# Kernel optimization log

Measured on AMD Instinct MI355X. Metric: run time of the kernel, lower is better.

## Reference

```python
import jax, jax.numpy as jnp
import numpy as np

H = 64  # rnn_size == input_size

def setup_inputs() -> dict:
    key = jax.random.key(0)
    ks = jax.random.split(key, 6)
    vocab = 32000
    B, T = 4096, 128
    s = 1.0 / np.sqrt(H)
    return {
        "inst": jax.random.randint(ks[0], (B, T), 0, vocab, dtype=jnp.int64),
        "embed_w": jax.random.normal(ks[1], (vocab + 1, H), dtype=jnp.float32),
        "W_ih": jax.random.uniform(ks[2], (4 * H, H), dtype=jnp.float32, minval=-s, maxval=s),
        "W_hh": jax.random.uniform(ks[3], (4 * H, H), dtype=jnp.float32, minval=-s, maxval=s),
        "b_ih": jax.random.uniform(ks[4], (4 * H,), dtype=jnp.float32, minval=-s, maxval=s),
        "b_hh": jax.random.uniform(ks[5], (4 * H,), dtype=jnp.float32, minval=-s, maxval=s),
    }

def _lstm_scan(xs, W_ih, W_hh, b_ih, b_hh):
    # xs: [T, B, H]. PyTorch LSTMCell gate order: i, f, g, o.
    B = xs.shape[1]
    # Precompute input projections for all timesteps in one big GEMM.
    x_proj = jnp.einsum('tbh,gh->tbg', xs, W_ih) + b_ih + b_hh  # [T, B, 4H]

    def step(carry, xp):
        h, c = carry
        gates = xp + h @ W_hh.T  # [B, 4H]
        i, f, g, o = jnp.split(gates, 4, axis=-1)
        c = jax.nn.sigmoid(f) * c + jax.nn.sigmoid(i) * jnp.tanh(g)
        h = jax.nn.sigmoid(o) * jnp.tanh(c)
        return (h, c), None

    h0 = jnp.zeros((B, H), dtype=xs.dtype)
    c0 = jnp.zeros((B, H), dtype=xs.dtype)
    (h, c), _ = jax.lax.scan(step, (h0, c0), x_proj)
    return h

def reference(inst, embed_w, W_ih, W_hh, b_ih, b_hh):
    # inst: [B, T] int; embedding lookup for whole sequence at once.
    xs = embed_w[inst]                 # [B, T, H]
    xs = jnp.swapaxes(xs, 0, 1)        # [T, B, H] for scan over time
    return _lstm_scan(xs, W_ih, W_hh, b_ih, b_hh)  # final h: [B, H]
```

## Files before the change

### kernel.cpp

```cpp
#include <hip/hip_runtime.h>
#include <hip/hip_bf16.h>

#define H_DIM   64
#define T_STEPS 128
#define B_TOT   4096
#define BB      8
#define SK      72
#define NTHREADS 256
#define XBATCH  8

typedef _Float16 half8  __attribute__((ext_vector_type(8)));
typedef __fp16   fp16x2 __attribute__((ext_vector_type(2)));
typedef __attribute__((ext_vector_type(4))) float f32x4;

#if __has_builtin(__builtin_amdgcn_exp2f)
#define EXP2(x) __builtin_amdgcn_exp2f(x)
#else
#define EXP2(x) exp2f(x)
#endif

__device__ __forceinline__ float sigmoid2(float xp) {
    return __builtin_amdgcn_rcpf(1.0f + EXP2(-xp));
}
__device__ __forceinline__ float tanh2(float xp) {
    return fmaf(-2.0f, __builtin_amdgcn_rcpf(EXP2(xp) + 1.0f), 1.0f);
}

__device__ __forceinline__ float xor8_dpp(float v) {
    return __int_as_float(__builtin_amdgcn_mov_dpp(
        __float_as_int(v), 0x128 , 0xf, 0xf, false));
}

__global__ __launch_bounds__(NTHREADS) void lstm_fused(
    const int* __restrict__ inst, const float* __restrict__ embed,
    const float* __restrict__ Wih, const float* __restrict__ Whh,
    const float* __restrict__ bih, const float* __restrict__ bhh,
    float* __restrict__ out)
{
    __shared__ __align__(16) _Float16 sX[2][16][SK];
    __shared__ __align__(16) _Float16 sH[2][16][SK];
    __shared__ int sInst[BB * T_STEPS];

    const int tid  = (int)threadIdx.x;
    const int w    = tid >> 6;
    const int l    = tid & 63;
    const int lrow = l & 15;
    const int lk   = l >> 4;
    const bool losd = (lrow < 8);
    const int colbase = w * 16 + (lrow & 7);
    const int rstar = losd ? 0 : 1;
    const int mrow  = lk * 4 + rstar;
    const int br    = lk * 2 + rstar;
    const int b0    = (int)blockIdx.x * BB;

    const float L2E     = 1.4426950408889634f;
    const float TWO_L2E = 2.8853900817779268f;

    for (int i = tid; i < BB * T_STEPS; i += NTHREADS)
        sInst[i] = inst[b0 * T_STEPS + i];

    for (int i = tid; i < 2 * 16 * SK; i += NTHREADS) {
        ((_Float16*)sX)[i] = (_Float16)0.0f;
        ((_Float16*)sH)[i] = (_Float16)0.0f;
    }
    __syncthreads();

    half8 wf[2][2][4];
    float bias[2][2];
#pragma unroll
    for (int cg = 0; cg < 2; ++cg) {
#pragma unroll
        for (int q = 0; q < 2; ++q) {
            const int gate = q * 2 + (lrow >> 3);
            const float ws = (gate == 2) ? TWO_L2E : L2E;
            const int gcol = gate * 64 + colbase + cg * 8;
            bias[cg][q] = (bih[gcol] + bhh[gcol]) * ws;
#pragma unroll
            for (int kf = 0; kf < 4; ++kf) {
                const float* src = (kf < 2 ? Wih : Whh) + (long)gcol * H_DIM + (kf & 1) * 32 + lk * 8;
                half8 v;
#pragma unroll
                for (int jj = 0; jj < 8; ++jj) v[jj] = (_Float16)(src[jj] * ws);
                wf[cg][q][kf] = v;
            }
        }
    }

    const int xr = tid >> 5;
    const int xc = tid & 31;
    const int xm = (xr >> 1) * 4 + (xr & 1);
    {
        const int idx = sInst[xr * T_STEPS + 0];
        const float2 xv = *reinterpret_cast<const float2*>(embed + (long)idx * H_DIM + xc * 2);
        fp16x2 hp = __builtin_amdgcn_cvt_pkrtz(xv.x, xv.y);
        *reinterpret_cast<fp16x2*>(&sX[0][xm][xc * 2]) = hp;
    }

    float2 xbuf[XBATCH];
#pragma unroll
    for (int j = 0; j < XBATCH; ++j) {
        const int idx = sInst[xr * T_STEPS + 1 + j];
        xbuf[j] = *reinterpret_cast<const float2*>(embed + (long)idx * H_DIM + xc * 2);
    }
    __syncthreads();

    float creg[2] = {0.f, 0.f};
    float hreg[2] = {0.f, 0.f};

    for (int tb = 0; tb < T_STEPS; tb += XBATCH) {
#pragma unroll
        for (int j = 0; j < XBATCH; ++j) {
            const int t   = tb + j;
            const int buf = j & 1;
            const int ob  = buf ^ 1;
            const bool pf = (t + 1 < T_STEPS);

            const float2 xcur = xbuf[j];

            if (j == XBATCH - 1 && pf) {
#pragma unroll
                for (int jj = 0; jj < XBATCH; ++jj) {
                    const int tt = t + 2 + jj;
                    if (tt < T_STEPS) {
                        const int idx = sInst[xr * T_STEPS + tt];
                        xbuf[jj] = *reinterpret_cast<const float2*>(embed + (long)idx * H_DIM + xc * 2);
                    }
                }
            }

            half8 a0 = *reinterpret_cast<const half8*>(&sX[buf][lrow][lk * 8]);
            half8 a1 = *reinterpret_cast<const half8*>(&sX[buf][lrow][32 + lk * 8]);
            half8 a2 = *reinterpret_cast<const half8*>(&sH[buf][lrow][lk * 8]);
            half8 a3 = *reinterpret_cast<const half8*>(&sH[buf][lrow][32 + lk * 8]);

            f32x4 acc[2][2];
#pragma unroll
            for (int cg = 0; cg < 2; ++cg) {
#pragma unroll
                for (int q = 0; q < 2; ++q) {
                    f32x4 a = {bias[cg][q], bias[cg][q], bias[cg][q], bias[cg][q]};
                    a = __builtin_amdgcn_mfma_f32_16x16x32_f16(a0, wf[cg][q][0], a, 0, 0, 0);
                    a = __builtin_amdgcn_mfma_f32_16x16x32_f16(a1, wf[cg][q][1], a, 0, 0, 0);
                    a = __builtin_amdgcn_mfma_f32_16x16x32_f16(a2, wf[cg][q][2], a, 0, 0, 0);
                    a = __builtin_amdgcn_mfma_f32_16x16x32_f16(a3, wf[cg][q][3], a, 0, 0, 0);
                    acc[cg][q] = a;
                }
            }

#pragma unroll
            for (int cg = 0; cg < 2; ++cg) {
                const float loc0 = losd ? acc[cg][0][0] : acc[cg][0][1];
                const float loc1 = losd ? acc[cg][1][0] : acc[cg][1][1];
                const float rem0 = xor8_dpp(losd ? acc[cg][0][1] : acc[cg][0][0]);
                const float rem1 = xor8_dpp(losd ? acc[cg][1][1] : acc[cg][1][0]);
                const float vi = losd ? loc0 : rem0;
                const float vf = losd ? rem0 : loc0;
                const float vg = losd ? loc1 : rem1;
                const float vo = losd ? rem1 : loc1;

                const float iv = sigmoid2(vi);
                const float fv = sigmoid2(vf);
                const float gv = tanh2(vg);
                const float ov = sigmoid2(vo);
                const float g2 = gv * TWO_L2E;
                const float cs = fmaf(fv, creg[cg], iv * g2);
                creg[cg] = cs;
                hreg[cg] = ov * tanh2(cs);

                if (pf)
                    sH[ob][mrow][colbase + cg * 8] = (_Float16)hreg[cg];
            }

            if (pf) {
                fp16x2 hp = __builtin_amdgcn_cvt_pkrtz(xcur.x, xcur.y);
                *reinterpret_cast<fp16x2*>(&sX[ob][xm][xc * 2]) = hp;
            }
            __syncthreads();
        }
    }

    out[(long)(b0 + br) * H_DIM + colbase]     = hreg[0];
    out[(long)(b0 + br) * H_DIM + colbase + 8] = hreg[1];
}

extern "C" void kernel_launch(void* const* d_in, const int* in_sizes, int n_in,
                              void* d_out, int out_size, void* d_ws, size_t ws_size,
                              hipStream_t stream) {
    const int*   inst  = (const int*)  d_in[0];
    const float* embed = (const float*)d_in[1];
    const float* Wih   = (const float*)d_in[2];
    const float* Whh   = (const float*)d_in[3];
    const float* bih   = (const float*)d_in[4];
    const float* bhh   = (const float*)d_in[5];
    float* out = (float*)d_out;

    lstm_fused<<<B_TOT / BB, NTHREADS, 0, stream>>>(inst, embed, Wih, Whh, bih, bhh, out);
}
```

Before: 99.53 us.

## Split LSTM gate columns across eight waves instead of four

Doubles the block to 512 threads so each wave owns 8 hidden columns instead of 16, halving per-wave MFMA and activation work per timestep and the weight registers held per lane. The embedding gather is remapped so each wave loads one batch row as one float per lane. This shortens each serial recurrent step's critical path, at the cost of a larger workgroup barrier every step and scalar rather than float2 global loads.

```diff
diff --git a/kernel.cpp b/kernel.cpp
--- a/kernel.cpp
+++ b/kernel.cpp
@@ -6,11 +6,10 @@
 #define B_TOT   4096
 #define BB      8
 #define SK      72
-#define NTHREADS 256
+#define NTHREADS 512
 #define XBATCH  8
 
 typedef _Float16 half8  __attribute__((ext_vector_type(8)));
-typedef __fp16   fp16x2 __attribute__((ext_vector_type(2)));
 typedef __attribute__((ext_vector_type(4))) float f32x4;
 
 #if __has_builtin(__builtin_amdgcn_exp2f)
@@ -31,7 +30,7 @@
         __float_as_int(v), 0x128 , 0xf, 0xf, false));
 }
 
-__global__ __launch_bounds__(NTHREADS) void lstm_fused(
+__global__ __launch_bounds__(NTHREADS, 4) void lstm_fused(
     const int* __restrict__ inst, const float* __restrict__ embed,
     const float* __restrict__ Wih, const float* __restrict__ Whh,
     const float* __restrict__ bih, const float* __restrict__ bhh,
@@ -47,7 +46,7 @@
     const int lrow = l & 15;
     const int lk   = l >> 4;
     const bool losd = (lrow < 8);
-    const int colbase = w * 16 + (lrow & 7);
+    const int col   = w * 8 + (lrow & 7);
     const int rstar = losd ? 0 : 1;
     const int mrow  = lk * 4 + rstar;
     const int br    = lk * 2 + rstar;
@@ -65,47 +64,39 @@
     }
     __syncthreads();
 
-    half8 wf[2][2][4];
-    float bias[2][2];
+    half8 wf[2][4];
+    float bias[2];
 #pragma unroll
-    for (int cg = 0; cg < 2; ++cg) {
+    for (int q = 0; q < 2; ++q) {
+        const int gate = q * 2 + (lrow >> 3);
+        const float ws = (gate == 2) ? TWO_L2E : L2E;
+        const int gcol = gate * 64 + col;
+        bias[q] = (bih[gcol] + bhh[gcol]) * ws;
 #pragma unroll
-        for (int q = 0; q < 2; ++q) {
-            const int gate = q * 2 + (lrow >> 3);
-            const float ws = (gate == 2) ? TWO_L2E : L2E;
-            const int gcol = gate * 64 + colbase + cg * 8;
-            bias[cg][q] = (bih[gcol] + bhh[gcol]) * ws;
+        for (int kf = 0; kf < 4; ++kf) {
+            const float* src = (kf < 2 ? Wih : Whh) + (long)gcol * H_DIM + (kf & 1) * 32 + lk * 8;
+            half8 v;
 #pragma unroll
-            for (int kf = 0; kf < 4; ++kf) {
-                const float* src = (kf < 2 ? Wih : Whh) + (long)gcol * H_DIM + (kf & 1) * 32 + lk * 8;
-                half8 v;
-#pragma unroll
-                for (int jj = 0; jj < 8; ++jj) v[jj] = (_Float16)(src[jj] * ws);
-                wf[cg][q][kf] = v;
-            }
+            for (int jj = 0; jj < 8; ++jj) v[jj] = (_Float16)(src[jj] * ws);
+            wf[q][kf] = v;
         }
     }
 
-    const int xr = tid >> 5;
-    const int xc = tid & 31;
-    const int xm = (xr >> 1) * 4 + (xr & 1);
+    const int xmw = (w >> 1) * 4 + (w & 1);
     {
-        const int idx = sInst[xr * T_STEPS + 0];
-        const float2 xv = *reinterpret_cast<const float2*>(embed + (long)idx * H_DIM + xc * 2);
-        fp16x2 hp = __builtin_amdgcn_cvt_pkrtz(xv.x, xv.y);
-        *reinterpret_cast<fp16x2*>(&sX[0][xm][xc * 2]) = hp;
+        const int idx = sInst[w * T_STEPS + 0];
+        sX[0][xmw][l] = (_Float16)embed[(long)idx * H_DIM + l];
     }
 
-    float2 xbuf[XBATCH];
+    float xbuf[XBATCH];
 #pragma unroll
     for (int j = 0; j < XBATCH; ++j) {
-        const int idx = sInst[xr * T_STEPS + 1 + j];
-        xbuf[j] = *reinterpret_cast<const float2*>(embed + (long)idx * H_DIM + xc * 2);
+        const int idx = sInst[w * T_STEPS + 1 + j];
+        xbuf[j] = embed[(long)idx * H_DIM + l];
     }
     __syncthreads();
 
-    float creg[2] = {0.f, 0.f};
-    float hreg[2] = {0.f, 0.f};
+    float creg = 0.f, hreg = 0.f;
 
     for (int tb = 0; tb < T_STEPS; tb += XBATCH) {
 #pragma unroll
@@ -115,15 +106,15 @@
             const int ob  = buf ^ 1;
             const bool pf = (t + 1 < T_STEPS);
 
-            const float2 xcur = xbuf[j];
+            const float xcur = xbuf[j];
 
             if (j == XBATCH - 1 && pf) {
 #pragma unroll
                 for (int jj = 0; jj < XBATCH; ++jj) {
                     const int tt = t + 2 + jj;
                     if (tt < T_STEPS) {
-                        const int idx = sInst[xr * T_STEPS + tt];
-                        xbuf[jj] = *reinterpret_cast<const float2*>(embed + (long)idx * H_DIM + xc * 2);
+                        const int idx = sInst[w * T_STEPS + tt];
+                        xbuf[jj] = embed[(long)idx * H_DIM + l];
                     }
                 }
             }
@@ -133,54 +124,41 @@
             half8 a2 = *reinterpret_cast<const half8*>(&sH[buf][lrow][lk * 8]);
             half8 a3 = *reinterpret_cast<const half8*>(&sH[buf][lrow][32 + lk * 8]);
 
-            f32x4 acc[2][2];
+            f32x4 acc[2];
 #pragma unroll
-            for (int cg = 0; cg < 2; ++cg) {
-#pragma unroll
-                for (int q = 0; q < 2; ++q) {
-                    f32x4 a = {bias[cg][q], bias[cg][q], bias[cg][q], bias[cg][q]};
-                    a = __builtin_amdgcn_mfma_f32_16x16x32_f16(a0, wf[cg][q][0], a, 0, 0, 0);
-                    a = __builtin_amdgcn_mfma_f32_16x16x32_f16(a1, wf[cg][q][1], a, 0, 0, 0);
-                    a = __builtin_amdgcn_mfma_f32_16x16x32_f16(a2, wf[cg][q][2], a, 0, 0, 0);
-                    a = __builtin_amdgcn_mfma_f32_16x16x32_f16(a3, wf[cg][q][3], a, 0, 0, 0);
-                    acc[cg][q] = a;
-                }
+            for (int q = 0; q < 2; ++q) {
+                f32x4 a = {bias[q], bias[q], bias[q], bias[q]};
+                a = __builtin_amdgcn_mfma_f32_16x16x32_f16(a0, wf[q][0], a, 0, 0, 0);
+                a = __builtin_amdgcn_mfma_f32_16x16x32_f16(a1, wf[q][1], a, 0, 0, 0);
+                a = __builtin_amdgcn_mfma_f32_16x16x32_f16(a2, wf[q][2], a, 0, 0, 0);
+                a = __builtin_amdgcn_mfma_f32_16x16x32_f16(a3, wf[q][3], a, 0, 0, 0);
+                acc[q] = a;
             }
 
-#pragma unroll
-            for (int cg = 0; cg < 2; ++cg) {
-                const float loc0 = losd ? acc[cg][0][0] : acc[cg][0][1];
-                const float loc1 = losd ? acc[cg][1][0] : acc[cg][1][1];
-                const float rem0 = xor8_dpp(losd ? acc[cg][0][1] : acc[cg][0][0]);
-                const float rem1 = xor8_dpp(losd ? acc[cg][1][1] : acc[cg][1][0]);
-                const float vi = losd ? loc0 : rem0;
-                const float vf = losd ? rem0 : loc0;
-                const float vg = losd ? loc1 : rem1;
-                const float vo = losd ? rem1 : loc1;
+            const float recv0 = xor8_dpp(losd ? acc[0][1] : acc[0][0]);
+            const float recv1 = xor8_dpp(losd ? acc[1][1] : acc[1][0]);
+            const float vi = losd ? acc[0][0] : recv0;
+            const float vf = losd ? recv0     : acc[0][1];
+            const float vg = losd ? acc[1][0] : recv1;
+            const float vo = losd ? recv1     : acc[1][1];
 
-                const float iv = sigmoid2(vi);
-                const float fv = sigmoid2(vf);
-                const float gv = tanh2(vg);
-                const float ov = sigmoid2(vo);
-                const float g2 = gv * TWO_L2E;
-                const float cs = fmaf(fv, creg[cg], iv * g2);
-                creg[cg] = cs;
-                hreg[cg] = ov * tanh2(cs);
-
-                if (pf)
-                    sH[ob][mrow][colbase + cg * 8] = (_Float16)hreg[cg];
-            }
+            const float iv = sigmoid2(vi);
+            const float fv = sigmoid2(vf);
+            const float gv = tanh2(vg);
+            const float ov = sigmoid2(vo);
+            const float cs = fmaf(fv, creg, iv * (gv * TWO_L2E));
+            creg = cs;
+            hreg = ov * tanh2(cs);
 
             if (pf) {
-                fp16x2 hp = __builtin_amdgcn_cvt_pkrtz(xcur.x, xcur.y);
-                *reinterpret_cast<fp16x2*>(&sX[ob][xm][xc * 2]) = hp;
+                sH[ob][mrow][col] = (_Float16)hreg;
+                sX[ob][xmw][l]    = (_Float16)xcur;
             }
             __syncthreads();
         }
     }
 
-    out[(long)(b0 + br) * H_DIM + colbase]     = hreg[0];
-    out[(long)(b0 + br) * H_DIM + colbase + 8] = hreg[1];
+    out[(long)(b0 + br) * H_DIM + col] = hreg;
 }
 
 extern "C" void kernel_launch(void* const* d_in, const int* in_sizes, int n_in,
```

Result: faster. 80.96 us (-18.7%).
